# Kernel tuning notes

Hardware: AMD Instinct MI355X
Metric: run time of the kernel (lower is better)

## Reference

```python
import jax, jax.numpy as jnp
import numpy as np

B, S, H, NH, NKV, HD, E, I = 1, 2048, 1024, 16, 8, 64, 8, 2048
TOPK = 2
EPS = 1e-6
THETA = 1e6


def setup_inputs() -> dict:
    key = jax.random.key(0)
    ks = jax.random.split(key, 12)
    init = lambda k, shp: jax.random.normal(k, shp, jnp.float32) * 0.02
    hidden_states = jax.random.normal(ks[0], (B, S, H), jnp.float32)
    attention_mask = jnp.ones((B, S), jnp.float32)
    position_ids = jnp.broadcast_to(jnp.arange(S, dtype=jnp.int32), (B, S))
    inv_freq = 1.0 / (THETA ** (jnp.arange(0, HD, 2, dtype=jnp.float32) / HD))
    freqs = jnp.outer(jnp.arange(S, dtype=jnp.float32), inv_freq)  # [S, HD/2]
    emb = jnp.concatenate([freqs, freqs], axis=-1)                  # [S, HD]
    return dict(
        hidden_states=hidden_states,
        attention_mask=attention_mask,
        position_ids=position_ids,
        sin=jnp.sin(emb), cos=jnp.cos(emb),
        wq=init(ks[1], (H, NH * HD)),
        wk=init(ks[2], (H, NKV * HD)),
        wv=init(ks[3], (H, NKV * HD)),
        wo=init(ks[4], (NH * HD, H)),
        ln1=jnp.ones((H,), jnp.float32),
        ln2=jnp.ones((H,), jnp.float32),
        gate_w=init(ks[5], (H, E)),
        w1=init(ks[6], (E, H, I)),
        w3=init(ks[7], (E, H, I)),
        w2=init(ks[8], (E, I, H)),
    )


def _rms_norm(x, w):
    return x * jax.lax.rsqrt(jnp.mean(jnp.square(x), -1, keepdims=True) + EPS) * w


def _rotate_half(x):
    h = x.shape[-1] // 2
    return jnp.concatenate([-x[..., h:], x[..., :h]], axis=-1)


def reference(hidden_states, attention_mask, position_ids, sin, cos,
              wq, wk, wv, wo, ln1, ln2, gate_w, w1, w3, w2):
    x = hidden_states
    # ---- self-attention block ----
    h = _rms_norm(x, ln1)
    q = (h @ wq).reshape(B, S, NH, HD).transpose(0, 2, 1, 3)    # [B,NH,S,HD]
    k = (h @ wk).reshape(B, S, NKV, HD).transpose(0, 2, 1, 3)   # [B,NKV,S,HD]
    v = (h @ wv).reshape(B, S, NKV, HD).transpose(0, 2, 1, 3)
    sb = sin[position_ids][:, None]  # [B,1,S,HD]
    cb = cos[position_ids][:, None]
    q = q * cb + _rotate_half(q) * sb
    k = k * cb + _rotate_half(k) * sb
    rep = NH // NKV
    k = jnp.repeat(k, rep, axis=1)  # GQA repeat -> [B,NH,S,HD]
    v = jnp.repeat(v, rep, axis=1)
    causal = jnp.tril(jnp.ones((S, S), bool))
    mask = causal[None, None] & (attention_mask[:, None, None, :] > 0)
    bias = jnp.where(mask, 0.0, jnp.finfo(jnp.float32).min)
    scale = 1.0 / jnp.sqrt(jnp.float32(HD))
    scores = jnp.einsum('bhqd,bhkd->bhqk', q, k) * scale + bias
    attn = jax.nn.softmax(scores, axis=-1)
    o = jnp.einsum('bhqk,bhkd->bhqd', attn, v)
    o = o.transpose(0, 2, 1, 3).reshape(B, S, NH * HD) @ wo
    x = x + o
    # ---- sparse MoE block (top-2 of E experts, SiLU-gated MLP) ----
    t = _rms_norm(x, ln2).reshape(B * S, H)
    router_logits = t @ gate_w                         # [T,E]
    probs = jax.nn.softmax(router_logits, axis=-1)
    top_w, top_i = jax.lax.top_k(probs, TOPK)          # [T,2]
    top_w = top_w / jnp.sum(top_w, axis=-1, keepdims=True)
    full_w = jnp.sum(jax.nn.one_hot(top_i, E, dtype=t.dtype) * top_w[..., None], axis=1)  # [T,E]
    moe_out = jnp.zeros_like(t)
    for e in range(E):  # fixed small expert count
        ge = jax.nn.silu(t @ w1[e]) * (t @ w3[e])      # [T,I]
        moe_out = moe_out + full_w[:, e:e + 1] * (ge @ w2[e])
    x = x + moe_out.reshape(B, S, H)
    return x
```

## Files before the change

### kernel.cpp

```cpp
#include <hip/hip_runtime.h>

#define S 2048
#define H 1024
#define NH 16
#define NKV 8
#define HD 64
#define NE 8
#define ID 2048

typedef short bf16x8 __attribute__((ext_vector_type(8)));
typedef short bf16x4 __attribute__((ext_vector_type(4)));
typedef float f32x4 __attribute__((ext_vector_type(4)));

__device__ __forceinline__ unsigned short f2bf(float f) {
  unsigned u = __builtin_bit_cast(unsigned, f);
  u += 0x7FFFu + ((u >> 16) & 1u);
  return (unsigned short)(u >> 16);
}
__device__ __forceinline__ float bf2f(unsigned short h) {
  unsigned u = ((unsigned)h) << 16;
  return __builtin_bit_cast(float, u);
}
__device__ __forceinline__ unsigned cvtpk(float a, float b) {
  unsigned r;
  asm("v_cvt_pk_bf16_f32 %0, %1, %2" : "=v"(r) : "v"(a), "v"(b));
  return r;
}

typedef const __attribute__((address_space(1))) unsigned int gas_u32;
typedef __attribute__((address_space(3))) unsigned int las_u32;
__device__ __forceinline__ void gload16(const unsigned short* g, unsigned short* l) {
  __builtin_amdgcn_global_load_lds((gas_u32*)g, (las_u32*)l, 16, 0, 0);
}

__global__ __launch_bounds__(256) void rmsnorm_kernel(const float* __restrict__ x,
                                                      const float* __restrict__ wgt,
                                                      unsigned short* __restrict__ ohi,
                                                      unsigned short* __restrict__ olo) {
  int row = blockIdx.x;
  const float* xr = x + (size_t)row * H;
  int tid = threadIdx.x;
  float v[4];
  float ss = 0.f;
#pragma unroll
  for (int i = 0; i < 4; i++) {
    v[i] = xr[tid + i * 256];
    ss += v[i] * v[i];
  }
#pragma unroll
  for (int off = 1; off < 64; off <<= 1) ss += __shfl_xor(ss, off);
  __shared__ float part[4];
  if ((tid & 63) == 0) part[tid >> 6] = ss;
  __syncthreads();
  float tot = part[0] + part[1] + part[2] + part[3];
  float r = rsqrtf(tot * (1.f / H) + 1e-6f);
#pragma unroll
  for (int i = 0; i < 4; i++) {
    int c = tid + i * 256;
    float vv = v[i] * r * wgt[c];
    size_t o = (size_t)row * H + c;
    unsigned short h_ = f2bf(vv);
    ohi[o] = h_;
    olo[o] = f2bf(vv - bf2f(h_));
  }
}

__global__ __launch_bounds__(256) void rmsnorm_router_kernel(
    const float* __restrict__ x, const float* __restrict__ wgt,
    const float* __restrict__ gw, unsigned short* __restrict__ ohi,
    int* __restrict__ selE, float* __restrict__ selW) {
  int row = blockIdx.x;
  const float* xr = x + (size_t)row * H;
  int tid = threadIdx.x;
  float v[4];
  float ss = 0.f;
#pragma unroll
  for (int i = 0; i < 4; i++) {
    v[i] = xr[tid + i * 256];
    ss += v[i] * v[i];
  }
#pragma unroll
  for (int off = 1; off < 64; off <<= 1) ss += __shfl_xor(ss, off);
  __shared__ float part[4];
  __shared__ float red[4][NE];
  if ((tid & 63) == 0) part[tid >> 6] = ss;
  __syncthreads();
  float tot = part[0] + part[1] + part[2] + part[3];
  float r = rsqrtf(tot * (1.f / H) + 1e-6f);
  float acc[NE];
#pragma unroll
  for (int e = 0; e < NE; e++) acc[e] = 0.f;
#pragma unroll
  for (int i = 0; i < 4; i++) {
    int c = tid + i * 256;
    float vv = v[i] * r * wgt[c];
    ohi[(size_t)row * H + c] = f2bf(vv);
    const float4* gp = (const float4*)(gw + (size_t)c * NE);
    float4 g0 = gp[0], g1 = gp[1];
    acc[0] += vv * g0.x;
    acc[1] += vv * g0.y;
    acc[2] += vv * g0.z;
    acc[3] += vv * g0.w;
    acc[4] += vv * g1.x;
    acc[5] += vv * g1.y;
    acc[6] += vv * g1.z;
    acc[7] += vv * g1.w;
  }
#pragma unroll
  for (int off = 1; off < 64; off <<= 1) {
#pragma unroll
    for (int e = 0; e < NE; e++) acc[e] += __shfl_xor(acc[e], off);
  }
  if ((tid & 63) == 0) {
#pragma unroll
    for (int e = 0; e < NE; e++) red[tid >> 6][e] = acc[e];
  }
  __syncthreads();
  if (tid == 0) {
    float lg[NE];
#pragma unroll
    for (int e = 0; e < NE; e++) lg[e] = red[0][e] + red[1][e] + red[2][e] + red[3][e];
    int e1 = 0;
#pragma unroll
    for (int e = 1; e < NE; e++)
      if (lg[e] > lg[e1]) e1 = e;
    int e2 = -1;
#pragma unroll
    for (int e = 0; e < NE; e++)
      if (e != e1 && (e2 < 0 || lg[e] > lg[e2])) e2 = e;
    float w1v = 1.f / (1.f + __expf(lg[e2] - lg[e1]));
    selE[row] = e1 | (e2 << 8);
    selW[row * 2] = w1v;
    selW[row * 2 + 1] = 1.f - w1v;
  }
}

__global__ __launch_bounds__(256) void assign_kernel(const int* __restrict__ selE,
                                                     int* __restrict__ cnt,
                                                     int* __restrict__ offs,
                                                     int* __restrict__ tmap,
                                                     int* __restrict__ idxb,
                                                     int* __restrict__ tokslot) {
  int tid = threadIdx.x;
  __shared__ int sc[256][NE];
  int pack[8];
  int hist[NE];
#pragma unroll
  for (int e = 0; e < NE; e++) hist[e] = 0;
#pragma unroll
  for (int i = 0; i < 8; i++) {
    pack[i] = selE[tid * 8 + i];
    hist[pack[i] & 255]++;
    hist[(pack[i] >> 8) & 255]++;
  }
#pragma unroll
  for (int e = 0; e < NE; e++) sc[tid][e] = hist[e];
  __syncthreads();
  for (int off = 1; off < 256; off <<= 1) {
    int add[NE];
    bool has = tid >= off;
    if (has) {
#pragma unroll
      for (int e = 0; e < NE; e++) add[e] = sc[tid - off][e];
    }
    __syncthreads();
    if (has) {
#pragma unroll
      for (int e = 0; e < NE; e++) sc[tid][e] += add[e];
    }
    __syncthreads();
  }
  int offsL[NE];
  {
    int a = 0;
#pragma unroll
    for (int e = 0; e < NE; e++) {
      offsL[e] = a;
      a += sc[255][e];
    }
  }
  if (tid == 0) {
    int t = 0;
    for (int e = 0; e < NE; e++) {
      int totE = sc[255][e];
      offs[e] = offsL[e];
      cnt[e] = totE;
      int nt = (totE + 127) >> 7;
      for (int i = 0; i < nt; i++) tmap[t++] = (e << 16) | i;
    }
    offs[NE] = offsL[NE - 1] + sc[255][NE - 1];
    tmap[63] = t;
  }
  int run[NE];
#pragma unroll
  for (int e = 0; e < NE; e++) run[e] = sc[tid][e] - hist[e];
#pragma unroll
  for (int i = 0; i < 8; i++) {
    int tok = tid * 8 + i;
    int e1 = pack[i] & 255, e2 = (pack[i] >> 8) & 255;
    int p1 = run[e1]++;
    idxb[e1 * S + p1] = tok;
    int p2 = run[e2]++;
    idxb[e2 * S + p2] = tok;
    tokslot[tok * 2] = offsL[e1] + p1;
    tokslot[tok * 2 + 1] = offsL[e2] + p2;
  }
}

__global__ __launch_bounds__(256) void moe_gather_kernel(const float* __restrict__ moeP,
                                                         const int* __restrict__ tokslot,
                                                         const float* __restrict__ selW,
                                                         float* __restrict__ out) {
  int tok = blockIdx.x;
  int c = threadIdx.x * 4;
  int s0 = tokslot[tok * 2], s1 = tokslot[tok * 2 + 1];
  float w0 = selW[tok * 2], w1 = selW[tok * 2 + 1];
  const float* P0 = moeP;
  const float* P1 = moeP + (size_t)4096 * 1024;
  float4 a0 = *(const float4*)(P0 + (size_t)s0 * 1024 + c);
  float4 b0 = *(const float4*)(P1 + (size_t)s0 * 1024 + c);
  float4 a1 = *(const float4*)(P0 + (size_t)s1 * 1024 + c);
  float4 b1 = *(const float4*)(P1 + (size_t)s1 * 1024 + c);
  float* op = out + (size_t)tok * 1024 + c;
  float4 o = *(float4*)op;
  o.x += w0 * (a0.x + b0.x) + w1 * (a1.x + b1.x);
  o.y += w0 * (a0.y + b0.y) + w1 * (a1.y + b1.y);
  o.z += w0 * (a0.z + b0.z) + w1 * (a1.z + b1.z);
  o.w += w0 * (a0.w + b0.w) + w1 * (a1.w + b1.w);
  *(float4*)op = o;
}

template <bool LO>
__global__ __launch_bounds__(256) void tconv_kernel(const float* __restrict__ src,
                                                    unsigned short* __restrict__ hi,
                                                    unsigned short* __restrict__ lo,
                                                    int K, int N, long long sStride,
                                                    long long dStride) {
  int nt = blockIdx.x, kt = blockIdx.y, b = blockIdx.z;
  src += (size_t)b * sStride;
  hi += (size_t)b * dStride;
  if (LO) lo += (size_t)b * dStride;
  __shared__ float tile[64][65];
  int tid = threadIdx.x;
  int r = tid >> 2, cs = (tid & 3) * 16;
  const float* s0 = src + (size_t)(kt * 64 + r) * N + nt * 64 + cs;
#pragma unroll
  for (int i = 0; i < 16; i += 4) {
    float4 a = *(const float4*)(s0 + i);
    tile[r][cs + i] = a.x;
    tile[r][cs + i + 1] = a.y;
    tile[r][cs + i + 2] = a.z;
    tile[r][cs + i + 3] = a.w;
  }
  __syncthreads();
  int n = nt * 64 + r;
  size_t dbase = (size_t)n * K + kt * 64 + cs;
  unsigned short th[16], tl[16];
#pragma unroll
  for (int i = 0; i < 16; i++) {
    float vv = tile[cs + i][r];
    unsigned short h_ = f2bf(vv);
    th[i] = h_;
    if (LO) tl[i] = f2bf(vv - bf2f(h_));
  }
  *(bf16x8*)(hi + dbase) = *(bf16x8*)&th[0];
  *(bf16x8*)(hi + dbase + 8) = *(bf16x8*)&th[8];
  if (LO) {
    *(bf16x8*)(lo + dbase) = *(bf16x8*)&tl[0];
    *(bf16x8*)(lo + dbase + 8) = *(bf16x8*)&tl[8];
  }
}

template <int MODE>
__global__ __launch_bounds__(256, 4) void gemm_kernel(
    const unsigned short* __restrict__ Ah, const unsigned short* __restrict__ Al,
    const unsigned short* __restrict__ Bh, const unsigned short* __restrict__ Bl,
    float* __restrict__ C, float* __restrict__ C2, unsigned short* __restrict__ Gout,
    const float* __restrict__ resid, const int* __restrict__ idx,
    const int* __restrict__ cnt, const int* __restrict__ offs,
    const int* __restrict__ tmap, int N, int K) {
  constexpr int BM = (MODE <= 1) ? 64 : 128;
  constexpr int NI = BM / 32;
  int n0 = blockIdx.x * 64, m0, e = 0;
  int ce = 0, gbase = 0;
  if (MODE >= 2) {
    int ntiles = tmap[63];
    if ((int)blockIdx.y >= ntiles) return;
    int packed = tmap[blockIdx.y];
    e = packed >> 16;
    m0 = (packed & 0xffff) * 128;
    ce = cnt[e];
    gbase = offs[e];
  } else {
    m0 = blockIdx.y * BM;
  }
  const unsigned short* bhp = Bh;
  const unsigned short* blp = Bl;
  if (MODE == 2) {
    bhp += (size_t)e * 2048 * 1024;
    blp += (size_t)e * 2048 * 1024;
  }
  if (MODE == 3) bhp += (size_t)e * 1024 * 2048;

  __shared__ __align__(16) unsigned short tAh[BM * 64];
  __shared__ __align__(16) unsigned short tAl[MODE <= 1 ? BM * 64 : 8];
  __shared__ __align__(16) unsigned short tBh[64 * 64];
  __shared__ __align__(16) unsigned short tBl[MODE <= 2 ? 64 * 64 : 8];

  int tid = threadIdx.x, w = tid >> 6, lane = tid & 63;
  int lr = lane & 15, g = lane >> 4;
  int rloc = lane >> 3, slotg = (lane & 7) ^ rloc;
  int wm = w >> 1, wn = w & 1;

  unsigned aOff[NI], bOff[2];
#pragma unroll
  for (int cc = 0; cc < NI; cc++) {
    int rr = (w * NI + cc) * 8 + rloc;
    if (MODE == 2) {
      int gr = m0 + rr;
      if (gr > ce - 1) gr = ce - 1;
      int tok = idx[e * S + gr];
      aOff[cc] = (unsigned)(tok * K + slotg * 8);
    } else if (MODE == 3) {
      int gr = gbase + m0 + rr;
      if (gr > 4095) gr = 4095;
      aOff[cc] = (unsigned)(gr * K + slotg * 8);
    } else {
      aOff[cc] = (unsigned)((m0 + rr) * K + slotg * 8);
    }
  }
#pragma unroll
  for (int cc = 0; cc < 2; cc++) {
    int rr = (w * 2 + cc) * 8 + rloc;
    bOff[cc] = (unsigned)((n0 + rr) * K + slotg * 8);
  }

  f32x4 acc[NI][2], acc2[NI][2];
#pragma unroll
  for (int i = 0; i < NI; i++)
#pragma unroll
    for (int j = 0; j < 2; j++) {
      acc[i][j] = f32x4{0.f, 0.f, 0.f, 0.f};
      if (MODE == 2) acc2[i][j] = f32x4{0.f, 0.f, 0.f, 0.f};
    }

  int kbeg = 0, kend = K;
  if (MODE == 3) {
    kbeg = (int)blockIdx.z * (K >> 1);
    kend = kbeg + (K >> 1);
  }
  for (int k0 = kbeg; k0 < kend; k0 += 64) {
    __syncthreads();
#pragma unroll
    for (int cc = 0; cc < NI; cc++) {
      int cb = (w * NI + cc) * 512;
      gload16(Ah + aOff[cc] + k0, &tAh[cb]);
      if (MODE <= 1) gload16(Al + aOff[cc] + k0, &tAl[cb]);
    }
#pragma unroll
    for (int cc = 0; cc < 2; cc++) {
      int cb = (w * 2 + cc) * 512;
      gload16(bhp + bOff[cc] + k0, &tBh[cb]);
      if (MODE <= 2) gload16(blp + bOff[cc] + k0, &tBl[cb]);
    }
    __syncthreads();
    bf16x8 fah[NI][2], fal[NI][2];
#pragma unroll
    for (int i = 0; i < NI; i++) {
      int ar = wm * (BM / 2) + i * 16 + lr;
#pragma unroll
      for (int kk = 0; kk < 2; kk++) {
        int off = ar * 64 + (((kk * 4 + g) ^ (ar & 7)) * 8);
        fah[i][kk] = *(const bf16x8*)&tAh[off];
        if (MODE <= 1) fal[i][kk] = *(const bf16x8*)&tAl[off];
      }
    }
#pragma unroll
    for (int j = 0; j < 2; j++) {
      int br = wn * 32 + j * 16 + lr;
      bf16x8 fbh[2], fbl[2];
#pragma unroll
      for (int kk = 0; kk < 2; kk++) {
        int off = br * 64 + (((kk * 4 + g) ^ (br & 7)) * 8);
        fbh[kk] = *(const bf16x8*)&tBh[off];
        if (MODE <= 2) fbl[kk] = *(const bf16x8*)&tBl[off];
      }
#pragma unroll
      for (int i = 0; i < NI; i++) {
#pragma unroll
        for (int kk = 0; kk < 2; kk++) {
          acc[i][j] = __builtin_amdgcn_mfma_f32_16x16x32_bf16(fah[i][kk], fbh[kk], acc[i][j], 0, 0, 0);
          if (MODE <= 1) {
            acc[i][j] = __builtin_amdgcn_mfma_f32_16x16x32_bf16(fah[i][kk], fbl[kk], acc[i][j], 0, 0, 0);
            acc[i][j] = __builtin_amdgcn_mfma_f32_16x16x32_bf16(fal[i][kk], fbh[kk], acc[i][j], 0, 0, 0);
          }
          if (MODE == 2)
            acc2[i][j] = __builtin_amdgcn_mfma_f32_16x16x32_bf16(fah[i][kk], fbl[kk], acc2[i][j], 0, 0, 0);
        }
      }
    }
  }
#pragma unroll
  for (int i = 0; i < NI; i++)
#pragma unroll
    for (int j = 0; j < 2; j++)
#pragma unroll
      for (int r = 0; r < 4; r++) {
        int grow = wm * (BM / 2) + i * 16 + g * 4 + r;
        int gcol = n0 + wn * 32 + j * 16 + lr;
        float v = acc[i][j][r];
        if (MODE == 0) {
          C[(size_t)(m0 + grow) * N + gcol] = v;
        } else if (MODE == 1) {
          float o = v + resid[(size_t)(m0 + grow) * N + gcol];
          C[(size_t)(m0 + grow) * N + gcol] = o;
          C2[(size_t)(m0 + grow) * N + gcol] = o;
        } else if (MODE == 2) {
          if (m0 + grow < ce) {
            float g3 = acc2[i][j][r];
            float sg = v / (1.f + __expf(-v));
            Gout[(size_t)(gbase + m0 + grow) * 2048 + gcol] = f2bf(sg * g3);
          }
        } else {
          if (m0 + grow < ce) {
            C[(size_t)blockIdx.z * 4096 * 1024 + (size_t)(gbase + m0 + grow) * 1024 + gcol] = v;
          }
        }
      }
}

__global__ __launch_bounds__(256) void rope_kernel(
    const float* __restrict__ qkv, const float* __restrict__ sinb,
    const float* __restrict__ cosb, const int* __restrict__ pos,
    unsigned short* __restrict__ qhi, unsigned short* __restrict__ qlo,
    unsigned short* __restrict__ khi, unsigned short* __restrict__ klo) {
  int i = blockIdx.x * 256 + threadIdx.x;
  int d = i & 31;
  int s = (i >> 5) & 2047;
  int hh = i >> 16;
  int p = pos[s];
  float c0 = cosb[p * HD + d], c1 = cosb[p * HD + d + 32];
  float s0 = sinb[p * HD + d], s1 = sinb[p * HD + d + 32];
  const float* srcb = qkv + (size_t)s * 2048;
  if (hh < NH) {
    float x0 = srcb[hh * HD + d], x1 = srcb[hh * HD + d + 32];
    float r0 = (x0 * c0 - x1 * s0) * 0.125f;
    float r1 = (x1 * c1 + x0 * s1) * 0.125f;
    size_t o = ((size_t)hh * S + s) * HD + d;
    unsigned short h0 = f2bf(r0), h1 = f2bf(r1);
    qhi[o] = h0;
    qlo[o] = f2bf(r0 - bf2f(h0));
    qhi[o + 32] = h1;
    qlo[o + 32] = f2bf(r1 - bf2f(h1));
  } else {
    int hk = hh - NH;
    float x0 = srcb[1024 + hk * HD + d], x1 = srcb[1024 + hk * HD + d + 32];
    float r0 = x0 * c0 - x1 * s0;
    float r1 = x1 * c1 + x0 * s1;
    size_t o = ((size_t)hk * S + s) * HD + d;
    unsigned short h0 = f2bf(r0), h1 = f2bf(r1);
    khi[o] = h0;
    klo[o] = f2bf(r0 - bf2f(h0));
    khi[o + 32] = h1;
    klo[o + 32] = f2bf(r1 - bf2f(h1));
  }
}

__global__ __launch_bounds__(256) void vtrans_kernel(const float* __restrict__ qkv,
                                                     unsigned short* __restrict__ vThi,
                                                     unsigned short* __restrict__ vTlo) {
  int st = blockIdx.x, hk = blockIdx.y;
  __shared__ float tile[64][65];
  int tid = threadIdx.x;
  int r = tid >> 2, seg = (tid & 3) * 16;
  const float* src = qkv + (size_t)(st * 64 + r) * 2048 + 1536 + hk * HD + seg;
#pragma unroll
  for (int i = 0; i < 16; i += 4) {
    float4 a = *(const float4*)(src + i);
    tile[r][seg + i] = a.x;
    tile[r][seg + i + 1] = a.y;
    tile[r][seg + i + 2] = a.z;
    tile[r][seg + i + 3] = a.w;
  }
  __syncthreads();
  int d = tid >> 2, ss = (tid & 3) * 16;
  unsigned short th[16], tl[16];
#pragma unroll
  for (int i = 0; i < 16; i++) {
    float vv = tile[ss + i][d];
    unsigned short h_ = f2bf(vv);
    th[i] = h_;
    tl[i] = f2bf(vv - bf2f(h_));
  }
  size_t dst = ((size_t)hk * HD + d) * S + st * 64 + ss;
  *(bf16x8*)(vThi + dst) = *(bf16x8*)&th[0];
  *(bf16x8*)(vThi + dst + 8) = *(bf16x8*)&th[8];
  *(bf16x8*)(vTlo + dst) = *(bf16x8*)&tl[0];
  *(bf16x8*)(vTlo + dst + 8) = *(bf16x8*)&tl[8];
}

#define FSWZ(row, byteoff) ((byteoff) ^ (((row) & 7) << 4))

__global__ __launch_bounds__(256, 4) void flash_kernel(
    const unsigned short* __restrict__ qhi, const unsigned short* __restrict__ qlo,
    const unsigned short* __restrict__ khip, const unsigned short* __restrict__ klop,
    const unsigned short* __restrict__ vthip, const unsigned short* __restrict__ vtlop,
    const float* __restrict__ amask, float* __restrict__ po, float* __restrict__ pm,
    float* __restrict__ pl) {
  int u = blockIdx.x;
  int r_ = u >> 8, base = u & 255;
  int qt = (base + r_ * 8) & 31;
  int head = ((base >> 5) & 7) | ((r_ & 1) << 3);
  int z = r_ >> 1;
  int tid = threadIdx.x;
  int w = tid >> 6, lane = tid & 63;
  int lr = lane & 15, g = lane >> 4;
  int rloc = lane >> 3, slotg = (lane & 7) ^ rloc;

  __shared__ __align__(16) unsigned short Khi[64 * 64];
  __shared__ __align__(16) unsigned short Klo[64 * 64];
  __shared__ __align__(16) unsigned short Vhi[64 * 64];
  __shared__ __align__(16) unsigned short Vlo[64 * 64];
  __shared__ __align__(16) unsigned short Pbuf[4][16 * 64];

  int qrow = qt * 64 + w * 16 + lr;
  bf16x8 qh[2], ql[2];
  {
    const unsigned short* qb = qhi + ((size_t)head * S + qrow) * HD;
    const unsigned short* qb2 = qlo + ((size_t)head * S + qrow) * HD;
    qh[0] = *(const bf16x8*)(qb + g * 8);
    qh[1] = *(const bf16x8*)(qb + 32 + g * 8);
    ql[0] = *(const bf16x8*)(qb2 + g * 8);
    ql[1] = *(const bf16x8*)(qb2 + 32 + g * 8);
  }

  f32x4 oacc[4];
#pragma unroll
  for (int dg = 0; dg < 4; dg++) oacc[dg] = f32x4{0.f, 0.f, 0.f, 0.f};
  float m = -1e30f, l = 0.f;

  const unsigned short* kbh = khip + (size_t)(head >> 1) * S * HD;
  const unsigned short* kbl = klop + (size_t)(head >> 1) * S * HD;
  const unsigned short* vbh = vthip + (size_t)(head >> 1) * HD * S;
  const unsigned short* vbl = vtlop + (size_t)(head >> 1) * HD * S;
  char* pbase = (char*)Pbuf[w];

  int nblk = qt + 1;
  int b0 = (z * nblk) >> 1, b1 = ((z + 1) * nblk) >> 1;

  for (int kb = b0; kb < b1; kb++) {
    int kv0 = kb * 64;
    __syncthreads();
#pragma unroll
    for (int cc = 0; cc < 2; cc++) {
      int c = w * 2 + cc;
      int r = c * 8 + rloc;
      gload16(kbh + (size_t)(kv0 + r) * HD + slotg * 8, &Khi[c * 512]);
      gload16(kbl + (size_t)(kv0 + r) * HD + slotg * 8, &Klo[c * 512]);
      gload16(vbh + (size_t)r * S + kv0 + slotg * 8, &Vhi[c * 512]);
      gload16(vbl + (size_t)r * S + kv0 + slotg * 8, &Vlo[c * 512]);
    }
    unsigned long long vm = __ballot(amask[kv0 + lane] > 0.f);
    __syncthreads();

    f32x4 sacc[4];
#pragma unroll
    for (int c = 0; c < 4; c++) sacc[c] = f32x4{0.f, 0.f, 0.f, 0.f};
#pragma unroll
    for (int c = 0; c < 4; c++) {
#pragma unroll
      for (int kc = 0; kc < 2; kc++) {
        int row = c * 16 + lr;
        int bo = FSWZ(row, row * 128 + kc * 64 + g * 16);
        bf16x8 khf = *(const bf16x8*)((char*)Khi + bo);
        bf16x8 klf = *(const bf16x8*)((char*)Klo + bo);
        sacc[c] = __builtin_amdgcn_mfma_f32_16x16x32_bf16(khf, qh[kc], sacc[c], 0, 0, 0);
        sacc[c] = __builtin_amdgcn_mfma_f32_16x16x32_bf16(khf, ql[kc], sacc[c], 0, 0, 0);
        sacc[c] = __builtin_amdgcn_mfma_f32_16x16x32_bf16(klf, qh[kc], sacc[c], 0, 0, 0);
      }
    }
    int qloc = w * 16 + lr;
    bool diag = (kb == qt);
    bool fullvis = (vm == ~0ull) && !diag;
    float tm = -1e30f;
    if (fullvis) {
#pragma unroll
      for (int c = 0; c < 4; c++)
#pragma unroll
        for (int r = 0; r < 4; r++) tm = fmaxf(tm, sacc[c][r]);
    } else {
#pragma unroll
      for (int c = 0; c < 4; c++) {
#pragma unroll
        for (int r = 0; r < 4; r++) {
          int kvloc = c * 16 + 4 * g + r;
          bool vis = ((vm >> kvloc) & 1ull) && (!diag || kvloc <= qloc);
          float sv = vis ? sacc[c][r] : -1e30f;
          sacc[c][r] = sv;
          tm = fmaxf(tm, sv);
        }
      }
    }
    tm = fmaxf(tm, __shfl_xor(tm, 16));
    tm = fmaxf(tm, __shfl_xor(tm, 32));
    bool skip = __all(tm - m <= 8.f);
    float newm = skip ? m : fmaxf(m, tm);
    float rs = 0.f;
#pragma unroll
    for (int c = 0; c < 4; c++) {
#pragma unroll
      for (int r = 0; r < 4; r++) {
        float p = __expf(sacc[c][r] - newm);
        sacc[c][r] = p;
        rs += p;
      }
    }
    rs += __shfl_xor(rs, 16);
    rs += __shfl_xor(rs, 32);
    if (!skip) {
      float alpha = __expf(m - newm);
      m = newm;
      l = l * alpha + rs;
#pragma unroll
      for (int dg = 0; dg < 4; dg++) {
#pragma unroll
        for (int r = 0; r < 4; r++) oacc[dg][r] *= alpha;
      }
    } else {
      l += rs;
    }
    unsigned hw[4][2];
#pragma unroll
    for (int c = 0; c < 4; c++) {
      hw[c][0] = cvtpk(sacc[c][0], sacc[c][1]);
      hw[c][1] = cvtpk(sacc[c][2], sacc[c][3]);
      uint2 hv = {hw[c][0], hw[c][1]};
      *(uint2*)(pbase + FSWZ(lr, lr * 128 + (c * 16 + 4 * g) * 2)) = hv;
    }
    bf16x8 pbh[2], pbl[2];
#pragma unroll
    for (int kc = 0; kc < 2; kc++)
      pbh[kc] = *(const bf16x8*)(pbase + FSWZ(lr, lr * 128 + kc * 64 + g * 16));
#pragma unroll
    for (int c = 0; c < 4; c++) {
      float h0 = __builtin_bit_cast(float, hw[c][0] << 16);
      float h1 = __builtin_bit_cast(float, hw[c][0] & 0xffff0000u);
      float h2 = __builtin_bit_cast(float, hw[c][1] << 16);
      float h3 = __builtin_bit_cast(float, hw[c][1] & 0xffff0000u);
      uint2 lv = {cvtpk(sacc[c][0] - h0, sacc[c][1] - h1),
                  cvtpk(sacc[c][2] - h2, sacc[c][3] - h3)};
      *(uint2*)(pbase + FSWZ(lr, lr * 128 + (c * 16 + 4 * g) * 2)) = lv;
    }
#pragma unroll
    for (int kc = 0; kc < 2; kc++)
      pbl[kc] = *(const bf16x8*)(pbase + FSWZ(lr, lr * 128 + kc * 64 + g * 16));
#pragma unroll
    for (int dg = 0; dg < 4; dg++) {
#pragma unroll
      for (int kc = 0; kc < 2; kc++) {
        int row = dg * 16 + lr;
        int bo = FSWZ(row, row * 128 + kc * 64 + g * 16);
        bf16x8 vhf = *(const bf16x8*)((char*)Vhi + bo);
        bf16x8 vlf = *(const bf16x8*)((char*)Vlo + bo);
        oacc[dg] = __builtin_amdgcn_mfma_f32_16x16x32_bf16(vhf, pbh[kc], oacc[dg], 0, 0, 0);
        oacc[dg] = __builtin_amdgcn_mfma_f32_16x16x32_bf16(vhf, pbl[kc], oacc[dg], 0, 0, 0);
        oacc[dg] = __builtin_amdgcn_mfma_f32_16x16x32_bf16(vlf, pbh[kc], oacc[dg], 0, 0, 0);
      }
    }
  }

  size_t pb = (size_t)(qt * 16 + head) * 2 + z;
  int row = w * 16 + lr;
  if (g == 0) {
    pm[pb * 64 + row] = m;
    pl[pb * 64 + row] = l;
  }
  float* pob = po + pb * 4096 + (size_t)row * 64;
#pragma unroll
  for (int dg = 0; dg < 4; dg++) {
    float4 v4 = {oacc[dg][0], oacc[dg][1], oacc[dg][2], oacc[dg][3]};
    *(float4*)(pob + dg * 16 + 4 * g) = v4;
  }
}

__global__ __launch_bounds__(256) void combine_kernel(const float* __restrict__ po,
                                                      const float* __restrict__ pm,
                                                      const float* __restrict__ pl,
                                                      unsigned short* __restrict__ ohi,
                                                      unsigned short* __restrict__ olo) {
  int qt = blockIdx.x, head = blockIdx.y;
  int r = threadIdx.x >> 2, dg = (threadIdx.x & 3) * 16;
  size_t base = (size_t)(qt * 16 + head) * 2;
  float m0v = pm[base * 64 + r], m1v = pm[(base + 1) * 64 + r];
  float l0 = pl[base * 64 + r], l1 = pl[(base + 1) * 64 + r];
  float M = fmaxf(m0v, m1v);
  float w0 = __expf(m0v - M), w1 = __expf(m1v - M);
  float inv = 1.f / (w0 * l0 + w1 * l1);
  const float* p0 = po + base * 4096 + (size_t)r * 64 + dg;
  const float* p1 = po + (base + 1) * 4096 + (size_t)r * 64 + dg;
  unsigned short th[16], tl[16];
#pragma unroll
  for (int i = 0; i < 16; i += 4) {
    float4 a = *(const float4*)(p0 + i);
    float4 b = *(const float4*)(p1 + i);
    float vv[4] = {(w0 * a.x + w1 * b.x) * inv, (w0 * a.y + w1 * b.y) * inv,
                   (w0 * a.z + w1 * b.z) * inv, (w0 * a.w + w1 * b.w) * inv};
#pragma unroll
    for (int j = 0; j < 4; j++) {
      unsigned short h_ = f2bf(vv[j]);
      th[i + j] = h_;
      tl[i + j] = f2bf(vv[j] - bf2f(h_));
    }
  }
  size_t ob = (size_t)(qt * 64 + r) * 1024 + head * 64 + dg;
  *(bf16x8*)(ohi + ob) = *(bf16x8*)&th[0];
  *(bf16x8*)(ohi + ob + 8) = *(bf16x8*)&th[8];
  *(bf16x8*)(olo + ob) = *(bf16x8*)&tl[0];
  *(bf16x8*)(olo + ob + 8) = *(bf16x8*)&tl[8];
}

extern "C" void kernel_launch(void* const* d_in, const int* in_sizes, int n_in,
                              void* d_out, int out_size, void* d_ws, size_t ws_size,
                              hipStream_t stream) {
  const float* x = (const float*)d_in[0];
  const float* amask = (const float*)d_in[1];
  const int* pos = (const int*)d_in[2];
  const float* sinb = (const float*)d_in[3];
  const float* cosb = (const float*)d_in[4];
  const float* wq = (const float*)d_in[5];
  const float* wk = (const float*)d_in[6];
  const float* wv = (const float*)d_in[7];
  const float* wo = (const float*)d_in[8];
  const float* ln1 = (const float*)d_in[9];
  const float* ln2 = (const float*)d_in[10];
  const float* gw = (const float*)d_in[11];
  const float* w1 = (const float*)d_in[12];
  const float* w3 = (const float*)d_in[13];
  const float* w2 = (const float*)d_in[14];
  float* out = (float*)d_out;

  char* ws = (char*)d_ws;
  const size_t MB = 1024 * 1024;
  float* x2 = (float*)(ws + 0 * MB);
  unsigned short* t_bf = (unsigned short*)(ws + 8 * MB);
  int* cnt = (int*)(ws + 12 * MB);
  int* offs = cnt + 16;
  int* tmap = cnt + 32;
  int* idxb = cnt + 128;
  int* selE = idxb + 16384;
  int* tokslot = selE + 2048;
  float* selW = (float*)(tokslot + 4096);
  unsigned short* G = (unsigned short*)(ws + 13 * MB);
  unsigned short* w1T = (unsigned short*)(ws + 29 * MB);
  unsigned short* w3T = (unsigned short*)(ws + 61 * MB);
  unsigned short* w2T = (unsigned short*)(ws + 29 * MB);
  float* moeP = (float*)(ws + 61 * MB);
  float* qkv = (float*)(ws + 13 * MB);
  float* po = (float*)(ws + 13 * MB);
  unsigned short* wqkvT_hi = (unsigned short*)(ws + 29 * MB);
  unsigned short* wqkvT_lo = (unsigned short*)(ws + 33 * MB);
  unsigned short* woT_hi = (unsigned short*)(ws + 37 * MB);
  unsigned short* woT_lo = (unsigned short*)(ws + 39 * MB);
  unsigned short* h_hi = (unsigned short*)(ws + 41 * MB);
  unsigned short* h_lo = (unsigned short*)(ws + 45 * MB);
  unsigned short* q_hi = (unsigned short*)(ws + 49 * MB);
  unsigned short* q_lo = (unsigned short*)(ws + 53 * MB);
  unsigned short* k_hi = (unsigned short*)(ws + 57 * MB);
  unsigned short* k_lo = (unsigned short*)(ws + 59 * MB);
  unsigned short* vT_hi = (unsigned short*)(ws + 61 * MB);
  unsigned short* vT_lo = (unsigned short*)(ws + 63 * MB);
  unsigned short* o_hi = (unsigned short*)(ws + 65 * MB);
  unsigned short* o_lo = (unsigned short*)(ws + 69 * MB);
  float* pm = (float*)(ws + 73 * MB);
  float* pl = (float*)(ws + 74 * MB);

  rmsnorm_kernel<<<S, 256, 0, stream>>>(x, ln1, h_hi, h_lo);
  tconv_kernel<true><<<dim3(16, 16, 1), 256, 0, stream>>>(wq, wqkvT_hi, wqkvT_lo, 1024, 1024, 0, 0);
  tconv_kernel<true><<<dim3(8, 16, 1), 256, 0, stream>>>(wk, wqkvT_hi + (size_t)1024 * 1024,
                                                         wqkvT_lo + (size_t)1024 * 1024, 1024, 512, 0, 0);
  tconv_kernel<true><<<dim3(8, 16, 1), 256, 0, stream>>>(wv, wqkvT_hi + (size_t)1536 * 1024,
                                                         wqkvT_lo + (size_t)1536 * 1024, 1024, 512, 0, 0);
  tconv_kernel<true><<<dim3(16, 16, 1), 256, 0, stream>>>(wo, woT_hi, woT_lo, 1024, 1024, 0, 0);

  gemm_kernel<0><<<dim3(32, 32, 1), 256, 0, stream>>>(h_hi, h_lo, wqkvT_hi, wqkvT_lo, qkv, nullptr,
                                                      nullptr, nullptr, nullptr, nullptr, nullptr,
                                                      nullptr, 2048, 1024);
  rope_kernel<<<6144, 256, 0, stream>>>(qkv, sinb, cosb, pos, q_hi, q_lo, k_hi, k_lo);
  vtrans_kernel<<<dim3(32, 8), 256, 0, stream>>>(qkv, vT_hi, vT_lo);
  flash_kernel<<<dim3(1024, 1, 1), 256, 0, stream>>>(q_hi, q_lo, k_hi, k_lo, vT_hi, vT_lo, amask,
                                                     po, pm, pl);
  combine_kernel<<<dim3(32, 16), 256, 0, stream>>>(po, pm, pl, o_hi, o_lo);
  gemm_kernel<1><<<dim3(16, 32, 1), 256, 0, stream>>>(o_hi, o_lo, woT_hi, woT_lo, x2, out, nullptr,
                                                      x, nullptr, nullptr, nullptr, nullptr, 1024,
                                                      1024);
  rmsnorm_router_kernel<<<S, 256, 0, stream>>>(x2, ln2, gw, t_bf, selE, selW);
  assign_kernel<<<1, 256, 0, stream>>>(selE, cnt, offs, tmap, idxb, tokslot);

  tconv_kernel<false><<<dim3(32, 16, 8), 256, 0, stream>>>(w1, w1T, nullptr, 1024, 2048,
                                                           (long long)1024 * 2048,
                                                           (long long)2048 * 1024);
  tconv_kernel<false><<<dim3(32, 16, 8), 256, 0, stream>>>(w3, w3T, nullptr, 1024, 2048,
                                                           (long long)1024 * 2048,
                                                           (long long)2048 * 1024);
  gemm_kernel<2><<<dim3(32, 40, 1), 256, 0, stream>>>(t_bf, nullptr, w1T, w3T, nullptr, nullptr, G,
                                                      nullptr, idxb, cnt, offs, tmap, 2048, 1024);
  tconv_kernel<false><<<dim3(16, 32, 8), 256, 0, stream>>>(w2, w2T, nullptr, 2048, 1024,
                                                           (long long)2048 * 1024,
                                                           (long long)1024 * 2048);
  gemm_kernel<3><<<dim3(16, 40, 2), 256, 0, stream>>>(G, nullptr, w2T, nullptr, moeP, nullptr,
                                                      nullptr, nullptr, idxb, cnt, offs, tmap, 1024,
                                                      2048);
  moe_gather_kernel<<<S, 256, 0, stream>>>(moeP, tokslot, selW, out);
}
```

Before: 300.0 us.

## Double-buffer K/V tiles in flash attention and split P hi/lo buffers

```diff
diff --git a/kernel.cpp b/kernel.cpp
--- a/kernel.cpp
+++ b/kernel.cpp
@@ -501,7 +501,7 @@
 
 #define FSWZ(row, byteoff) ((byteoff) ^ (((row) & 7) << 4))
 
-__global__ __launch_bounds__(256, 4) void flash_kernel(
+__global__ __launch_bounds__(256, 2) void flash_kernel(
     const unsigned short* __restrict__ qhi, const unsigned short* __restrict__ qlo,
     const unsigned short* __restrict__ khip, const unsigned short* __restrict__ klop,
     const unsigned short* __restrict__ vthip, const unsigned short* __restrict__ vtlop,
@@ -517,11 +517,12 @@
   int lr = lane & 15, g = lane >> 4;
   int rloc = lane >> 3, slotg = (lane & 7) ^ rloc;
 
-  __shared__ __align__(16) unsigned short Khi[64 * 64];
-  __shared__ __align__(16) unsigned short Klo[64 * 64];
-  __shared__ __align__(16) unsigned short Vhi[64 * 64];
-  __shared__ __align__(16) unsigned short Vlo[64 * 64];
-  __shared__ __align__(16) unsigned short Pbuf[4][16 * 64];
+  __shared__ __align__(16) unsigned short Khi[2][64 * 64];
+  __shared__ __align__(16) unsigned short Klo[2][64 * 64];
+  __shared__ __align__(16) unsigned short Vhi[2][64 * 64];
+  __shared__ __align__(16) unsigned short Vlo[2][64 * 64];
+  __shared__ __align__(16) unsigned short Phi[4][16 * 64];
+  __shared__ __align__(16) unsigned short Plo[4][16 * 64];
 
   int qrow = qt * 64 + w * 16 + lr;
   bf16x8 qh[2], ql[2];
@@ -543,25 +544,48 @@
   const unsigned short* kbl = klop + (size_t)(head >> 1) * S * HD;
   const unsigned short* vbh = vthip + (size_t)(head >> 1) * HD * S;
   const unsigned short* vbl = vtlop + (size_t)(head >> 1) * HD * S;
-  char* pbase = (char*)Pbuf[w];
+  char* phbase = (char*)Phi[w];
+  char* plbase = (char*)Plo[w];
 
   int nblk = qt + 1;
   int b0 = (z * nblk) >> 1, b1 = ((z + 1) * nblk) >> 1;
+  int sc = w * 2, sr0 = sc * 8 + rloc, sr1 = sr0 + 8;
+
+  if (b0 < b1) {
+    int kv0 = b0 * 64;
+    gload16(kbh + (size_t)(kv0 + sr0) * HD + slotg * 8, &Khi[0][sc * 512]);
+    gload16(kbh + (size_t)(kv0 + sr1) * HD + slotg * 8, &Khi[0][(sc + 1) * 512]);
+    gload16(kbl + (size_t)(kv0 + sr0) * HD + slotg * 8, &Klo[0][sc * 512]);
+    gload16(kbl + (size_t)(kv0 + sr1) * HD + slotg * 8, &Klo[0][(sc + 1) * 512]);
+    gload16(vbh + (size_t)sr0 * S + kv0 + slotg * 8, &Vhi[0][sc * 512]);
+    gload16(vbh + (size_t)sr1 * S + kv0 + slotg * 8, &Vhi[0][(sc + 1) * 512]);
+    gload16(vbl + (size_t)sr0 * S + kv0 + slotg * 8, &Vlo[0][sc * 512]);
+    gload16(vbl + (size_t)sr1 * S + kv0 + slotg * 8, &Vlo[0][(sc + 1) * 512]);
+  }
+  float am = (b0 < b1) ? amask[b0 * 64 + lane] : 0.f;
+  __syncthreads();
 
   for (int kb = b0; kb < b1; kb++) {
-    int kv0 = kb * 64;
-    __syncthreads();
-#pragma unroll
-    for (int cc = 0; cc < 2; cc++) {
-      int c = w * 2 + cc;
-      int r = c * 8 + rloc;
-      gload16(kbh + (size_t)(kv0 + r) * HD + slotg * 8, &Khi[c * 512]);
-      gload16(kbl + (size_t)(kv0 + r) * HD + slotg * 8, &Klo[c * 512]);
-      gload16(vbh + (size_t)r * S + kv0 + slotg * 8, &Vhi[c * 512]);
-      gload16(vbl + (size_t)r * S + kv0 + slotg * 8, &Vlo[c * 512]);
-    }
-    unsigned long long vm = __ballot(amask[kv0 + lane] > 0.f);
-    __syncthreads();
+    int buf = (kb - b0) & 1;
+    float am_next = 0.f;
+    if (kb + 1 < b1) {
+      int kv1 = (kb + 1) * 64;
+      int nb = buf ^ 1;
+      gload16(kbh + (size_t)(kv1 + sr0) * HD + slotg * 8, &Khi[nb][sc * 512]);
+      gload16(kbh + (size_t)(kv1 + sr1) * HD + slotg * 8, &Khi[nb][(sc + 1) * 512]);
+      gload16(kbl + (size_t)(kv1 + sr0) * HD + slotg * 8, &Klo[nb][sc * 512]);
+      gload16(kbl + (size_t)(kv1 + sr1) * HD + slotg * 8, &Klo[nb][(sc + 1) * 512]);
+      gload16(vbh + (size_t)sr0 * S + kv1 + slotg * 8, &Vhi[nb][sc * 512]);
+      gload16(vbh + (size_t)sr1 * S + kv1 + slotg * 8, &Vhi[nb][(sc + 1) * 512]);
+      gload16(vbl + (size_t)sr0 * S + kv1 + slotg * 8, &Vlo[nb][sc * 512]);
+      gload16(vbl + (size_t)sr1 * S + kv1 + slotg * 8, &Vlo[nb][(sc + 1) * 512]);
+      am_next = amask[kv1 + lane];
+    }
+    unsigned long long vm = __ballot(am > 0.f);
+    const char* khb = (const char*)Khi[buf];
+    const char* klb = (const char*)Klo[buf];
+    const char* vhb = (const char*)Vhi[buf];
+    const char* vlb = (const char*)Vlo[buf];
 
     f32x4 sacc[4];
 #pragma unroll
@@ -572,8 +596,8 @@
       for (int kc = 0; kc < 2; kc++) {
         int row = c * 16 + lr;
         int bo = FSWZ(row, row * 128 + kc * 64 + g * 16);
-        bf16x8 khf = *(const bf16x8*)((char*)Khi + bo);
-        bf16x8 klf = *(const bf16x8*)((char*)Klo + bo);
+        bf16x8 khf = *(const bf16x8*)(khb + bo);
+        bf16x8 klf = *(const bf16x8*)(klb + bo);
         sacc[c] = __builtin_amdgcn_mfma_f32_16x16x32_bf16(khf, qh[kc], sacc[c], 0, 0, 0);
         sacc[c] = __builtin_amdgcn_mfma_f32_16x16x32_bf16(khf, ql[kc], sacc[c], 0, 0, 0);
         sacc[c] = __builtin_amdgcn_mfma_f32_16x16x32_bf16(klf, qh[kc], sacc[c], 0, 0, 0);
@@ -635,12 +659,8 @@
       hw[c][0] = cvtpk(sacc[c][0], sacc[c][1]);
       hw[c][1] = cvtpk(sacc[c][2], sacc[c][3]);
       uint2 hv = {hw[c][0], hw[c][1]};
-      *(uint2*)(pbase + FSWZ(lr, lr * 128 + (c * 16 + 4 * g) * 2)) = hv;
-    }
-    bf16x8 pbh[2], pbl[2];
-#pragma unroll
-    for (int kc = 0; kc < 2; kc++)
-      pbh[kc] = *(const bf16x8*)(pbase + FSWZ(lr, lr * 128 + kc * 64 + g * 16));
+      *(uint2*)(phbase + FSWZ(lr, lr * 128 + (c * 16 + 4 * g) * 2)) = hv;
+    }
 #pragma unroll
     for (int c = 0; c < 4; c++) {
       float h0 = __builtin_bit_cast(float, hw[c][0] << 16);
@@ -649,24 +669,30 @@
       float h3 = __builtin_bit_cast(float, hw[c][1] & 0xffff0000u);
       uint2 lv = {cvtpk(sacc[c][0] - h0, sacc[c][1] - h1),
                   cvtpk(sacc[c][2] - h2, sacc[c][3] - h3)};
-      *(uint2*)(pbase + FSWZ(lr, lr * 128 + (c * 16 + 4 * g) * 2)) = lv;
-    }
-#pragma unroll
-    for (int kc = 0; kc < 2; kc++)
-      pbl[kc] = *(const bf16x8*)(pbase + FSWZ(lr, lr * 128 + kc * 64 + g * 16));
+      *(uint2*)(plbase + FSWZ(lr, lr * 128 + (c * 16 + 4 * g) * 2)) = lv;
+    }
+    bf16x8 pbh[2], pbl[2];
+#pragma unroll
+    for (int kc = 0; kc < 2; kc++) {
+      int bo = FSWZ(lr, lr * 128 + kc * 64 + g * 16);
+      pbh[kc] = *(const bf16x8*)(phbase + bo);
+      pbl[kc] = *(const bf16x8*)(plbase + bo);
+    }
 #pragma unroll
     for (int dg = 0; dg < 4; dg++) {
 #pragma unroll
       for (int kc = 0; kc < 2; kc++) {
         int row = dg * 16 + lr;
         int bo = FSWZ(row, row * 128 + kc * 64 + g * 16);
-        bf16x8 vhf = *(const bf16x8*)((char*)Vhi + bo);
-        bf16x8 vlf = *(const bf16x8*)((char*)Vlo + bo);
+        bf16x8 vhf = *(const bf16x8*)(vhb + bo);
+        bf16x8 vlf = *(const bf16x8*)(vlb + bo);
         oacc[dg] = __builtin_amdgcn_mfma_f32_16x16x32_bf16(vhf, pbh[kc], oacc[dg], 0, 0, 0);
         oacc[dg] = __builtin_amdgcn_mfma_f32_16x16x32_bf16(vhf, pbl[kc], oacc[dg], 0, 0, 0);
         oacc[dg] = __builtin_amdgcn_mfma_f32_16x16x32_bf16(vlf, pbh[kc], oacc[dg], 0, 0, 0);
       }
     }
+    am = am_next;
+    __syncthreads();
   }
 
   size_t pb = (size_t)(qt * 16 + head) * 2 + z;
```

Measured after the change: 313.4 us. 4.5% more time.
